# Kernel tuning notes

Hardware: AMD Instinct MI355X
Metric: run time of the kernel (lower is better)

Reference implementation:

```python
import jax, jax.numpy as jnp
import numpy as np

E = 8          # n_experts
K = 5          # n_active = int(0.7*E)
TEMP = float(np.e)

def _l2norm(v):
    n = jnp.linalg.norm(v, axis=-1, keepdims=True)
    return v / jnp.maximum(n, 1e-12)

def setup_inputs() -> dict:
    key = jax.random.key(0)
    ks = jax.random.split(key, 13)
    N, D, H, O = 4096, 2048, 4096, 2048
    s = lambda fan: 1.0 / np.sqrt(fan)
    return {
        "x":    jax.random.normal(ks[0], (N, D), jnp.float32),
        "Wg":   jax.random.normal(ks[1], (D, E), jnp.float32) * s(D),
        "bg":   jnp.zeros((E,), jnp.float32),
        "Wa":   jax.random.normal(ks[2], (D, 32), jnp.float32) * s(D),
        "ba":   jnp.zeros((32,), jnp.float32),
        "Wb":   jax.random.normal(ks[3], (32, 16), jnp.float32) * s(32),
        "bb":   jnp.zeros((16,), jnp.float32),
        "sigs": jax.random.normal(ks[4], (E, 16), jnp.float32) * 0.1,
        "W1":   jax.random.normal(ks[5], (E, D, H), jnp.float32) * s(D),
        "b1":   jnp.zeros((E, H), jnp.float32),
        "W2":   jax.random.normal(ks[6], (E, H, O), jnp.float32) * s(H),
        "b2":   jnp.zeros((E, O), jnp.float32),
    }

def reference(x, Wg, bg, Wa, ba, Wb, bb, sigs, W1, b1, W2, b2):
    # gating softmax (temperature = e)
    probs = jax.nn.softmax((x @ Wg + bg) / TEMP, axis=-1)          # [N, E]
    # PH feature match
    ph = jax.nn.relu(x @ Wa + ba) @ Wb + bb                        # [N, 16]
    ph_match = (_l2norm(ph) @ _l2norm(sigs).T + 1.0) / 2.0         # [N, E]
    effective = probs * ph_match                                   # [N, E]
    # top-k mask over experts
    _, idx = jax.lax.top_k(effective, K)                           # [N, K]
    mask = jnp.sum(jax.nn.one_hot(idx, E, dtype=effective.dtype), axis=-2)  # [N, E]
    weights = effective * mask
    weights = weights / (weights.sum(axis=-1, keepdims=True) + 1e-8)
    # dense all-expert FFN (eval mode: dropout is identity)
    h = jax.nn.relu(jnp.einsum('nd,edh->neh', x, W1) + b1)         # [N, E, H]
    outs = jnp.einsum('neh,eho->neo', h, W2) + b2                  # [N, E, O]
    return jnp.einsum('ne,neo->no', weights, outs)                 # [N, O]
```

## Files before the change

kernel.cpp:

```cpp
#include <hip/hip_runtime.h>
#include <hip/hip_bf16.h>
#include <stdint.h>

#define TOK  4096
#define DIM  2048
#define HID  4096
#define ODIM 2048
#define NEXP 8
#define KSEL 5

typedef __bf16 bf16x8 __attribute__((ext_vector_type(8)));
typedef float  f32x4  __attribute__((ext_vector_type(4)));
typedef unsigned short ushort8 __attribute__((ext_vector_type(8)));

__device__ __forceinline__ uint16_t f2bf(float f) {
  uint32_t u = __float_as_uint(f);
  u += 0x7FFFu + ((u >> 16) & 1u);
  return (uint16_t)(u >> 16);
}
__device__ __forceinline__ float bf2f(uint16_t h) {
  uint32_t u = ((uint32_t)h) << 16;
  return __uint_as_float(u);
}

#define GLD16(g, l) __builtin_amdgcn_global_load_lds(                      \
    (const __attribute__((address_space(1))) void*)(g),                    \
    (__attribute__((address_space(3))) void*)(l), 16, 0, 0)


__global__ void cast_x_kernel(const float* __restrict__ in,
                              uint16_t* __restrict__ out, int n4) {
  int i = blockIdx.x * blockDim.x + threadIdx.x;
  if (i >= n4) return;
  float4 v = ((const float4*)in)[i];
  ushort4 o;
  o.x = f2bf(v.x); o.y = f2bf(v.y); o.z = f2bf(v.z); o.w = f2bf(v.w);
  ((ushort4*)out)[i] = o;
}

__global__ void transpose_cast_kernel(const float* __restrict__ in,
                                      uint16_t* __restrict__ out,
                                      int R, int C, long inBatch, long outBatch) {
  __shared__ float tile[32][33];
  const float* src = in + (size_t)blockIdx.z * inBatch;
  uint16_t*    dst = out + (size_t)blockIdx.z * outBatch;
  int c0 = blockIdx.x * 32, r0 = blockIdx.y * 32;
  int tx = threadIdx.x, ty = threadIdx.y;
#pragma unroll
  for (int i = 0; i < 4; ++i)
    tile[ty + i * 8][tx] = src[(size_t)(r0 + ty + i * 8) * C + c0 + tx];
  __syncthreads();
#pragma unroll
  for (int i = 0; i < 4; ++i)
    dst[(size_t)(c0 + ty + i * 8) * R + r0 + tx] = f2bf(tile[tx][ty + i * 8]);
}


__global__ void routing_kernel(const float* __restrict__ x,
                               const float* __restrict__ Wg, const float* __restrict__ bg,
                               const float* __restrict__ Wa, const float* __restrict__ ba,
                               const float* __restrict__ Wb, const float* __restrict__ bb,
                               const float* __restrict__ sigs,
                               float* __restrict__ wts, int* __restrict__ selmask_g) {
  const int n    = blockIdx.x;
  const int lane = threadIdx.x;
  const float* xr = x + (size_t)n * DIM;

  float ga[NEXP]; float aa[32];
#pragma unroll
  for (int e = 0; e < NEXP; ++e) ga[e] = 0.f;
#pragma unroll
  for (int j = 0; j < 32; ++j) aa[j] = 0.f;

  for (int it = 0; it < DIM / 64; ++it) {
    int d = it * 64 + lane;
    float xv = xr[d];
    const float* wgr = Wg + (size_t)d * NEXP;
#pragma unroll
    for (int e = 0; e < NEXP; ++e) ga[e] += xv * wgr[e];
    const float* war = Wa + (size_t)d * 32;
#pragma unroll
    for (int j = 0; j < 32; ++j) aa[j] += xv * war[j];
  }
#pragma unroll
  for (int s = 1; s < 64; s <<= 1) {
#pragma unroll
    for (int e = 0; e < NEXP; ++e) ga[e] += __shfl_xor(ga[e], s);
#pragma unroll
    for (int j = 0; j < 32; ++j) aa[j] += __shfl_xor(aa[j], s);
  }

  float ph[16];
#pragma unroll
  for (int i = 0; i < 16; ++i) ph[i] = bb[i];
#pragma unroll
  for (int j = 0; j < 32; ++j) {
    float a = aa[j] + ba[j];
    a = a > 0.f ? a : 0.f;
#pragma unroll
    for (int i = 0; i < 16; ++i) ph[i] += a * Wb[j * 16 + i];
  }
  float nrm = 0.f;
#pragma unroll
  for (int i = 0; i < 16; ++i) nrm += ph[i] * ph[i];
  nrm = fmaxf(sqrtf(nrm), 1e-12f);

  const float invT = 0.36787944117144233f;
  float lg[NEXP], mx = -1e30f;
#pragma unroll
  for (int e = 0; e < NEXP; ++e) { lg[e] = (ga[e] + bg[e]) * invT; mx = fmaxf(mx, lg[e]); }
  float psum = 0.f, pr[NEXP];
#pragma unroll
  for (int e = 0; e < NEXP; ++e) { pr[e] = expf(lg[e] - mx); psum += pr[e]; }

  float eff[NEXP];
#pragma unroll
  for (int e = 0; e < NEXP; ++e) {
    const float* sg = sigs + e * 16;
    float dot = 0.f, sn = 0.f;
#pragma unroll
    for (int i = 0; i < 16; ++i) { dot += ph[i] * sg[i]; sn += sg[i] * sg[i]; }
    sn = fmaxf(sqrtf(sn), 1e-12f);
    float match = (dot / (nrm * sn) + 1.f) * 0.5f;
    eff[e] = (pr[e] / psum) * match;
  }

  int selmask = 0;
#pragma unroll
  for (int t = 0; t < KSEL; ++t) {
    int bi = 0; float bv = -1e30f;
#pragma unroll
    for (int e = 0; e < NEXP; ++e) {
      bool ok = !((selmask >> e) & 1);
      if (ok && eff[e] > bv) { bv = eff[e]; bi = e; }
    }
    selmask |= (1 << bi);
  }
  float wsum = 0.f, wv[NEXP];
#pragma unroll
  for (int e = 0; e < NEXP; ++e) {
    wv[e] = ((selmask >> e) & 1) ? eff[e] : 0.f;
    wsum += wv[e];
  }
  float inv = 1.f / (wsum + 1e-8f);
  if (lane == 0) {
#pragma unroll
    for (int e = 0; e < NEXP; ++e) wts[n * NEXP + e] = wv[e] * inv;
    selmask_g[n] = selmask;
  }
}


__global__ void listbuild_kernel(const int* __restrict__ selmask_g,
                                 const float* __restrict__ wts,
                                 int* __restrict__ cnt, int* __restrict__ base,
                                 int* __restrict__ list, int* __restrict__ slot_map,
                                 float* __restrict__ wrow) {
  const int e = blockIdx.x;
  const int t = threadIdx.x;
  __shared__ int cntT[256][NEXP];
  __shared__ int totAll[NEXP];
  __shared__ int sc[256];

  int msk[16];
  int c8[NEXP];
#pragma unroll
  for (int f = 0; f < NEXP; ++f) c8[f] = 0;
#pragma unroll
  for (int i = 0; i < 16; ++i) {
    msk[i] = selmask_g[t * 16 + i];
#pragma unroll
    for (int f = 0; f < NEXP; ++f) c8[f] += (msk[i] >> f) & 1;
  }
#pragma unroll
  for (int f = 0; f < NEXP; ++f) cntT[t][f] = c8[f];
  __syncthreads();

  if (t < NEXP) {
    int s = 0;
    for (int j = 0; j < 256; ++j) s += cntT[j][t];
    totAll[t] = s;
  }
  __syncthreads();

  if (e == 0 && t == 0) {
    int r = 0;
    for (int f = 0; f < NEXP; ++f) { cnt[f] = totAll[f]; base[f] = r; r += totAll[f]; }
  }
  int gbase = 0;
  for (int f = 0; f < e; ++f) gbase += totAll[f];

  sc[t] = c8[e];
  __syncthreads();
  for (int off = 1; off < 256; off <<= 1) {
    int v = (t >= off) ? sc[t - off] : 0;
    __syncthreads();
    sc[t] += v;
    __syncthreads();
  }
  int p = sc[t] - c8[e];

#pragma unroll
  for (int i = 0; i < 16; ++i) {
    const int n = t * 16 + i;
    const int m = msk[i];
    if ((m >> e) & 1) {
      list[e * TOK + p] = n;
      const int rank = __popc(m & ((1 << e) - 1));
      slot_map[n * KSEL + rank] = gbase + p;
      wrow[gbase + p] = wts[n * NEXP + e];
      ++p;
    }
  }
}


template <int MODE>
__launch_bounds__(512, 2)
__global__ void gemm_pipe_kernel(const uint16_t* __restrict__ A,
                                 const uint16_t* __restrict__ Bt,
                                 const int* __restrict__ cnt,
                                 const int* __restrict__ base,
                                 const int* __restrict__ list,
                                 const float* __restrict__ wrow,
                                 const float* __restrict__ bias,
                                 uint16_t* __restrict__ outb,
                                 int Kdim, int NTk, int Ncols) {
  __shared__ __attribute__((aligned(16))) uint16_t lds[4 * 16384];

  const int e  = blockIdx.z;
  const int ce = cnt[e];
  const int tileM = blockIdx.y * 256;
  if (tileM >= ce) return;
  const int be    = base[e];
  const int tileN = blockIdx.x * 256;
  const int tid = threadIdx.x, lane = tid & 63, wid = tid >> 6;
  const int wr = wid >> 2, wc = wid & 3;
  const int sr = (wid & 3) * 64 + lane;
  const int sg = wid >> 2;

  int pA = tileM + sr; pA = pA < ce ? pA : ce - 1;
  const uint16_t* aRow;
  if (MODE == 1) aRow = A + (size_t)list[e * TOK + pA] * Kdim;
  else           aRow = A + (size_t)(be + pA) * Kdim;
  const uint16_t* bRow = Bt + ((size_t)e * Ncols + tileN + sr) * Kdim;

  char* lbase = (char*)lds + wid * 1024;

#define STAGE_A(slotIdx, kOff)                                   \
  { char* lb = lbase + (slotIdx) * 32768;                        \
    GLD16(aRow + (kOff) + sg * 8,       lb);                     \
    GLD16(aRow + (kOff) + (2 + sg) * 8, lb + 8192); }
#define STAGE_B(slotIdx, kOff)                                   \
  { char* lb = lbase + (slotIdx) * 32768 + 16384;                \
    GLD16(bRow + (kOff) + sg * 8,       lb);                     \
    GLD16(bRow + (kOff) + (2 + sg) * 8, lb + 8192); }

  const int afrag = ((lane >> 4) << 8) + wr * 128 + (lane & 15);
  const int bfrag = ((lane >> 4) << 8) + wc * 64 + (lane & 15);

  f32x4 acc[8][4];
#pragma unroll
  for (int m = 0; m < 8; ++m)
#pragma unroll
    for (int n = 0; n < 4; ++n) acc[m][n] = (f32x4){0.f, 0.f, 0.f, 0.f};

  STAGE_A(0, 0);  STAGE_B(0, 0);
  STAGE_A(1, 32); STAGE_B(1, 32);
  STAGE_A(2, 64); STAGE_B(2, 64);

  for (int T = 0; T < NTk; ++T) {
    if (T + 2 < NTk)      asm volatile("s_waitcnt vmcnt(8)" ::: "memory");
    else if (T + 1 < NTk) asm volatile("s_waitcnt vmcnt(4)" ::: "memory");
    else                  asm volatile("s_waitcnt vmcnt(0)" ::: "memory");
    __builtin_amdgcn_sched_barrier(0);
    __builtin_amdgcn_s_barrier();

    const uint16_t* As = lds + (T & 3) * 16384;
    const uint16_t* Bs = As + 8192;
    const int kNext = (T + 3) * 32;
    const bool doStage = (T + 3) < NTk;

    bf16x8 av[8];
#pragma unroll
    for (int m = 0; m < 8; ++m)
      av[m] = *(const bf16x8*)(As + (size_t)(afrag + m * 16) * 8);
    bf16x8 bv0 = *(const bf16x8*)(Bs + (size_t)(bfrag + 0 * 16) * 8);
    bf16x8 bv1 = *(const bf16x8*)(Bs + (size_t)(bfrag + 1 * 16) * 8);
    if (doStage) STAGE_A((T + 3) & 3, kNext);
    __builtin_amdgcn_s_barrier();
    asm volatile("s_waitcnt lgkmcnt(0)" ::: "memory");
    __builtin_amdgcn_sched_barrier(0);
    __builtin_amdgcn_s_setprio(1);
#pragma unroll
    for (int m = 0; m < 8; ++m)
      acc[m][0] = __builtin_amdgcn_mfma_f32_16x16x32_bf16(av[m], bv0, acc[m][0], 0, 0, 0);
#pragma unroll
    for (int m = 0; m < 8; ++m)
      acc[m][1] = __builtin_amdgcn_mfma_f32_16x16x32_bf16(av[m], bv1, acc[m][1], 0, 0, 0);
    __builtin_amdgcn_s_setprio(0);

    bf16x8 bv2 = *(const bf16x8*)(Bs + (size_t)(bfrag + 2 * 16) * 8);
    bf16x8 bv3 = *(const bf16x8*)(Bs + (size_t)(bfrag + 3 * 16) * 8);
    if (doStage) STAGE_B((T + 3) & 3, kNext);
    __builtin_amdgcn_s_barrier();
    asm volatile("s_waitcnt lgkmcnt(0)" ::: "memory");
    __builtin_amdgcn_sched_barrier(0);
    __builtin_amdgcn_s_setprio(1);
#pragma unroll
    for (int m = 0; m < 8; ++m)
      acc[m][2] = __builtin_amdgcn_mfma_f32_16x16x32_bf16(av[m], bv2, acc[m][2], 0, 0, 0);
#pragma unroll
    for (int m = 0; m < 8; ++m)
      acc[m][3] = __builtin_amdgcn_mfma_f32_16x16x32_bf16(av[m], bv3, acc[m][3], 0, 0, 0);
    __builtin_amdgcn_s_setprio(0);
  }
#undef STAGE_A
#undef STAGE_B

  if (MODE == 1) {
    const float* b1e = bias + (size_t)e * Ncols;
#pragma unroll
    for (int m = 0; m < 8; ++m)
#pragma unroll
      for (int r = 0; r < 4; ++r) {
        const int p = tileM + wr * 128 + m * 16 + ((lane >> 4) << 2) + r;
        if (p < ce) {
          const float w = wrow[be + p];
          uint16_t* orow = outb + (size_t)(be + p) * Ncols;
#pragma unroll
          for (int n = 0; n < 4; ++n) {
            const int col = tileN + wc * 64 + n * 16 + (lane & 15);
            float v = acc[m][n][r] + b1e[col];
            v = v > 0.f ? v : 0.f;
            orow[col] = f2bf(v * w);
          }
        }
      }
  } else {
#pragma unroll
    for (int m = 0; m < 8; ++m)
#pragma unroll
      for (int r = 0; r < 4; ++r) {
        const int p = tileM + wr * 128 + m * 16 + ((lane >> 4) << 2) + r;
        if (p < ce) {
          uint16_t* orow = outb + (size_t)(be + p) * Ncols;
#pragma unroll
          for (int n = 0; n < 4; ++n) {
            const int col = tileN + wc * 64 + n * 16 + (lane & 15);
            orow[col] = f2bf(acc[m][n][r]);
          }
        }
      }
  }
}


__global__ void reduce_kernel(const uint16_t* __restrict__ obuf,
                              const int* __restrict__ slot_map,
                              const float* __restrict__ wts,
                              const float* __restrict__ b2,
                              float* __restrict__ out) {
  const int n = blockIdx.x;
  const int t = threadIdx.x;
  const int c = t * 8;

  int slots[KSEL];
#pragma unroll
  for (int k = 0; k < KSEL; ++k) slots[k] = slot_map[n * KSEL + k];
  float w8[NEXP];
#pragma unroll
  for (int e = 0; e < NEXP; ++e) w8[e] = wts[n * NEXP + e];

  float s[8];
#pragma unroll
  for (int j = 0; j < 8; ++j) s[j] = 0.f;
#pragma unroll
  for (int e = 0; e < NEXP; ++e) {
    const float4 b0 = *(const float4*)(b2 + (size_t)e * ODIM + c);
    const float4 b1v = *(const float4*)(b2 + (size_t)e * ODIM + c + 4);
    s[0] += w8[e] * b0.x; s[1] += w8[e] * b0.y; s[2] += w8[e] * b0.z; s[3] += w8[e] * b0.w;
    s[4] += w8[e] * b1v.x; s[5] += w8[e] * b1v.y; s[6] += w8[e] * b1v.z; s[7] += w8[e] * b1v.w;
  }
#pragma unroll
  for (int k = 0; k < KSEL; ++k) {
    const ushort8 v = *(const ushort8*)(obuf + (size_t)slots[k] * ODIM + c);
#pragma unroll
    for (int j = 0; j < 8; ++j) s[j] += bf2f(v[j]);
  }
  float4 o0 = make_float4(s[0], s[1], s[2], s[3]);
  float4 o1 = make_float4(s[4], s[5], s[6], s[7]);
  *(float4*)(out + (size_t)n * ODIM + c) = o0;
  *(float4*)(out + (size_t)n * ODIM + c + 4) = o1;
}


extern "C" void kernel_launch(void* const* d_in, const int* in_sizes, int n_in,
                              void* d_out, int out_size, void* d_ws, size_t ws_size,
                              hipStream_t stream) {
  const float* x    = (const float*)d_in[0];
  const float* Wg   = (const float*)d_in[1];
  const float* bg   = (const float*)d_in[2];
  const float* Wa   = (const float*)d_in[3];
  const float* ba   = (const float*)d_in[4];
  const float* Wb   = (const float*)d_in[5];
  const float* bb   = (const float*)d_in[6];
  const float* sigs = (const float*)d_in[7];
  const float* W1   = (const float*)d_in[8];
  const float* b1   = (const float*)d_in[9];
  const float* W2   = (const float*)d_in[10];
  const float* b2   = (const float*)d_in[11];
  float* out = (float*)d_out;

  char* ws = (char*)d_ws;
  float*    wts     = (float*)(ws + 0);
  int*      selmask = (int*)(ws + 131072);
  int*      cnt     = (int*)(ws + 147456);
  int*      base    = (int*)(ws + 147584);
  int*      slot_map= (int*)(ws + 151552);
  float*    wrow    = (float*)(ws + 233472);
  int*      list    = (int*)(ws + 315392);
  uint16_t* xbf     = (uint16_t*)(ws + 446464);
  uint16_t* W1T     = (uint16_t*)(ws + 17223680);
  uint16_t* W2T     = (uint16_t*)(ws + 151441408);
  uint16_t* hbuf    = (uint16_t*)(ws + 285659136);
  uint16_t* obuf    = (uint16_t*)(ws + 453431296);

  cast_x_kernel<<<(TOK * DIM / 4) / 256, 256, 0, stream>>>(x, xbf, TOK * DIM / 4);
  transpose_cast_kernel<<<dim3(HID / 32, DIM / 32, NEXP), dim3(32, 8), 0, stream>>>(
      W1, W1T, DIM, HID, (long)DIM * HID, (long)DIM * HID);
  transpose_cast_kernel<<<dim3(ODIM / 32, HID / 32, NEXP), dim3(32, 8), 0, stream>>>(
      W2, W2T, HID, ODIM, (long)HID * ODIM, (long)ODIM * HID);
  routing_kernel<<<TOK, 64, 0, stream>>>(x, Wg, bg, Wa, ba, Wb, bb, sigs, wts, selmask);
  listbuild_kernel<<<NEXP, 256, 0, stream>>>(selmask, wts, cnt, base, list, slot_map, wrow);

  gemm_pipe_kernel<1><<<dim3(HID / 256, 16, NEXP), 512, 0, stream>>>(
      xbf, W1T, cnt, base, list, wrow, b1, hbuf, DIM, DIM / 32, HID);
  gemm_pipe_kernel<2><<<dim3(ODIM / 256, 16, NEXP), 512, 0, stream>>>(
      hbuf, W2T, cnt, base, nullptr, nullptr, nullptr, obuf, HID, HID / 32, ODIM);
  reduce_kernel<<<TOK, 256, 0, stream>>>(obuf, slot_map, wts, b2, out);
}
```

Measured before the change: 1.529 ms.

## Shrink expert GEMM tiles to 128x128 with 256-thread blocks and one barrier

Changes the grouped expert GEMMs from 256x256 tiles with 8 waves to 128x128 tiles with 4 waves (each wave computes 64x64). All A and B staging for a K-step now happens in one combined STAGE, so the intra-iteration split and the extra barriers go away. Smaller tiles give more blocks, better tail handling for the ragged per-expert row counts, and lower LDS use. The cost is lower arithmetic intensity per LDS and global byte and more total global traffic for the operands.

```diff
diff --git a/kernel.cpp b/kernel.cpp
--- a/kernel.cpp
+++ b/kernel.cpp
@@ -216,7 +216,7 @@
 
 
 template <int MODE>
-__launch_bounds__(512, 2)
+__launch_bounds__(256, 2)
 __global__ void gemm_pipe_kernel(const uint16_t* __restrict__ A,
                                  const uint16_t* __restrict__ Bt,
                                  const int* __restrict__ cnt,
@@ -226,48 +226,50 @@
                                  const float* __restrict__ bias,
                                  uint16_t* __restrict__ outb,
                                  int Kdim, int NTk, int Ncols) {
-  __shared__ __attribute__((aligned(16))) uint16_t lds[4 * 16384];
+  __shared__ __attribute__((aligned(16))) uint16_t lds[4 * 8192];
 
   const int e  = blockIdx.z;
   const int ce = cnt[e];
-  const int tileM = blockIdx.y * 256;
+  const int tileM = blockIdx.y * 128;
   if (tileM >= ce) return;
   const int be    = base[e];
-  const int tileN = blockIdx.x * 256;
+  const int tileN = blockIdx.x * 128;
   const int tid = threadIdx.x, lane = tid & 63, wid = tid >> 6;
-  const int wr = wid >> 2, wc = wid & 3;
-  const int sr = (wid & 3) * 64 + lane;
-  const int sg = wid >> 2;
-
-  int pA = tileM + sr; pA = pA < ce ? pA : ce - 1;
+  const int wr = wid >> 1, wc = wid & 1;
+
+  const int srow = tid & 127;
+  const int g0   = tid >> 7;
+  int pA = tileM + srow; pA = pA < ce ? pA : ce - 1;
   const uint16_t* aRow;
   if (MODE == 1) aRow = A + (size_t)list[e * TOK + pA] * Kdim;
   else           aRow = A + (size_t)(be + pA) * Kdim;
-  const uint16_t* bRow = Bt + ((size_t)e * Ncols + tileN + sr) * Kdim;
-
-  char* lbase = (char*)lds + wid * 1024;
-
-#define STAGE_A(slotIdx, kOff)                                   \
-  { char* lb = lbase + (slotIdx) * 32768;                        \
-    GLD16(aRow + (kOff) + sg * 8,       lb);                     \
-    GLD16(aRow + (kOff) + (2 + sg) * 8, lb + 8192); }
-#define STAGE_B(slotIdx, kOff)                                   \
-  { char* lb = lbase + (slotIdx) * 32768 + 16384;                \
-    GLD16(bRow + (kOff) + sg * 8,       lb);                     \
-    GLD16(bRow + (kOff) + (2 + sg) * 8, lb + 8192); }
-
-  const int afrag = ((lane >> 4) << 8) + wr * 128 + (lane & 15);
-  const int bfrag = ((lane >> 4) << 8) + wc * 64 + (lane & 15);
-
-  f32x4 acc[8][4];
-#pragma unroll
-  for (int m = 0; m < 8; ++m)
+  const uint16_t* bRow = Bt + ((size_t)e * Ncols + tileN + srow) * Kdim;
+
+  char* ldsb = (char*)lds;
+  const uint32_t dA0 = (uint32_t)wid * 1024;
+  const uint32_t dA1 = dA0 + 4096;
+  const uint32_t dB0 = dA0 + 8192;
+  const uint32_t dB1 = dA0 + 12288;
+
+#define STAGE(slotIdx, kOff)                                              \
+  { const uint32_t sb = (uint32_t)(slotIdx) * 16384;                      \
+    GLD16(aRow + (kOff) + g0 * 8,       ldsb + sb + dA0);                 \
+    GLD16(aRow + (kOff) + (g0 + 2) * 8, ldsb + sb + dA1);                 \
+    GLD16(bRow + (kOff) + g0 * 8,       ldsb + sb + dB0);                 \
+    GLD16(bRow + (kOff) + (g0 + 2) * 8, ldsb + sb + dB1); }
+
+  const int afrag = ((lane >> 4) << 7) + wr * 64 + (lane & 15);
+  const int bfrag = ((lane >> 4) << 7) + wc * 64 + (lane & 15);
+
+  f32x4 acc[4][4];
+#pragma unroll
+  for (int m = 0; m < 4; ++m)
 #pragma unroll
     for (int n = 0; n < 4; ++n) acc[m][n] = (f32x4){0.f, 0.f, 0.f, 0.f};
 
-  STAGE_A(0, 0);  STAGE_B(0, 0);
-  STAGE_A(1, 32); STAGE_B(1, 32);
-  STAGE_A(2, 64); STAGE_B(2, 64);
+  STAGE(0, 0);
+  STAGE(1, 32);
+  STAGE(2, 64);
 
   for (int T = 0; T < NTk; ++T) {
     if (T + 2 < NTk)      asm volatile("s_waitcnt vmcnt(8)" ::: "memory");
@@ -276,55 +278,38 @@
     __builtin_amdgcn_sched_barrier(0);
     __builtin_amdgcn_s_barrier();
 
-    const uint16_t* As = lds + (T & 3) * 16384;
-    const uint16_t* Bs = As + 8192;
-    const int kNext = (T + 3) * 32;
-    const bool doStage = (T + 3) < NTk;
-
-    bf16x8 av[8];
-#pragma unroll
-    for (int m = 0; m < 8; ++m)
+    const uint16_t* As = lds + (T & 3) * 8192;
+    const uint16_t* Bs = As + 4096;
+
+    bf16x8 av[4], bv[4];
+#pragma unroll
+    for (int m = 0; m < 4; ++m)
       av[m] = *(const bf16x8*)(As + (size_t)(afrag + m * 16) * 8);
-    bf16x8 bv0 = *(const bf16x8*)(Bs + (size_t)(bfrag + 0 * 16) * 8);
-    bf16x8 bv1 = *(const bf16x8*)(Bs + (size_t)(bfrag + 1 * 16) * 8);
-    if (doStage) STAGE_A((T + 3) & 3, kNext);
-    __builtin_amdgcn_s_barrier();
+#pragma unroll
+    for (int n = 0; n < 4; ++n)
+      bv[n] = *(const bf16x8*)(Bs + (size_t)(bfrag + n * 16) * 8);
+
+    if (T + 3 < NTk) STAGE((T + 3) & 3, (T + 3) * 32);
+
     asm volatile("s_waitcnt lgkmcnt(0)" ::: "memory");
     __builtin_amdgcn_sched_barrier(0);
     __builtin_amdgcn_s_setprio(1);
 #pragma unroll
-    for (int m = 0; m < 8; ++m)
-      acc[m][0] = __builtin_amdgcn_mfma_f32_16x16x32_bf16(av[m], bv0, acc[m][0], 0, 0, 0);
-#pragma unroll
-    for (int m = 0; m < 8; ++m)
-      acc[m][1] = __builtin_amdgcn_mfma_f32_16x16x32_bf16(av[m], bv1, acc[m][1], 0, 0, 0);
+    for (int m = 0; m < 4; ++m)
+#pragma unroll
+      for (int n = 0; n < 4; ++n)
+        acc[m][n] = __builtin_amdgcn_mfma_f32_16x16x32_bf16(av[m], bv[n], acc[m][n], 0, 0, 0);
     __builtin_amdgcn_s_setprio(0);
-
-    bf16x8 bv2 = *(const bf16x8*)(Bs + (size_t)(bfrag + 2 * 16) * 8);
-    bf16x8 bv3 = *(const bf16x8*)(Bs + (size_t)(bfrag + 3 * 16) * 8);
-    if (doStage) STAGE_B((T + 3) & 3, kNext);
-    __builtin_amdgcn_s_barrier();
-    asm volatile("s_waitcnt lgkmcnt(0)" ::: "memory");
-    __builtin_amdgcn_sched_barrier(0);
-    __builtin_amdgcn_s_setprio(1);
-#pragma unroll
-    for (int m = 0; m < 8; ++m)
-      acc[m][2] = __builtin_amdgcn_mfma_f32_16x16x32_bf16(av[m], bv2, acc[m][2], 0, 0, 0);
-#pragma unroll
-    for (int m = 0; m < 8; ++m)
-      acc[m][3] = __builtin_amdgcn_mfma_f32_16x16x32_bf16(av[m], bv3, acc[m][3], 0, 0, 0);
-    __builtin_amdgcn_s_setprio(0);
-  }
-#undef STAGE_A
-#undef STAGE_B
+  }
+#undef STAGE
 
   if (MODE == 1) {
     const float* b1e = bias + (size_t)e * Ncols;
 #pragma unroll
-    for (int m = 0; m < 8; ++m)
+    for (int m = 0; m < 4; ++m)
 #pragma unroll
       for (int r = 0; r < 4; ++r) {
-        const int p = tileM + wr * 128 + m * 16 + ((lane >> 4) << 2) + r;
+        const int p = tileM + wr * 64 + m * 16 + ((lane >> 4) << 2) + r;
         if (p < ce) {
           const float w = wrow[be + p];
           uint16_t* orow = outb + (size_t)(be + p) * Ncols;
@@ -339,10 +324,10 @@
       }
   } else {
 #pragma unroll
-    for (int m = 0; m < 8; ++m)
+    for (int m = 0; m < 4; ++m)
 #pragma unroll
       for (int r = 0; r < 4; ++r) {
-        const int p = tileM + wr * 128 + m * 16 + ((lane >> 4) << 2) + r;
+        const int p = tileM + wr * 64 + m * 16 + ((lane >> 4) << 2) + r;
         if (p < ce) {
           uint16_t* orow = outb + (size_t)(be + p) * Ncols;
 #pragma unroll
@@ -434,9 +419,9 @@
   routing_kernel<<<TOK, 64, 0, stream>>>(x, Wg, bg, Wa, ba, Wb, bb, sigs, wts, selmask);
   listbuild_kernel<<<NEXP, 256, 0, stream>>>(selmask, wts, cnt, base, list, slot_map, wrow);
 
-  gemm_pipe_kernel<1><<<dim3(HID / 256, 16, NEXP), 512, 0, stream>>>(
+  gemm_pipe_kernel<1><<<dim3(HID / 128, TOK / 128, NEXP), 256, 0, stream>>>(
       xbf, W1T, cnt, base, list, wrow, b1, hbuf, DIM, DIM / 32, HID);
-  gemm_pipe_kernel<2><<<dim3(ODIM / 256, 16, NEXP), 512, 0, stream>>>(
+  gemm_pipe_kernel<2><<<dim3(ODIM / 128, TOK / 128, NEXP), 256, 0, stream>>>(
       hbuf, W2T, cnt, base, nullptr, nullptr, nullptr, obuf, HID, HID / 32, ODIM);
   reduce_kernel<<<TOK, 256, 0, stream>>>(obuf, slot_map, wts, b2, out);
 }
```

After: 1.920 ms. 1.26x slower.
